# Performance work log

Hardware: AMD Instinct MI355X
Metric: run time of the kernel (lower is better)

## Reference

```python
import jax, jax.numpy as jnp
import numpy as np
import math

SPARSITY = 0.5
EPS = 1e-5


def _quant(x, bit, after_relu):
    # mirrors torch quantize_per_tensor math; straight-through (torch mutates x.data)
    def q(x):
        mx, mn = x.max(), x.min()
        scale = (mx - mn) / (2 ** bit - 1)
        if after_relu:
            ir = jnp.clip(jnp.round(x / scale), 0.0, 2 ** bit - 1)
            return ir * scale
        zp_min = jnp.floor(mn / scale)
        return (jnp.round((x - mn) / scale) + zp_min) * scale
    return x + jax.lax.stop_gradient(q(x) - x)


def _subnet(scores, k):
    # GetSubnet: top-k mask of |scores| with straight-through gradient
    s = jnp.abs(scores)
    flat = s.ravel()
    j = int((1.0 - k) * flat.size)
    order = jnp.argsort(flat)
    mask = jnp.zeros_like(flat).at[order[j:]].set(1.0).reshape(s.shape)
    return jax.lax.stop_gradient(mask - s) + s


def _scale(hw_one, fan_in):
    std = math.sqrt(2.0) / math.sqrt(fan_in * 0.5)
    return hw_one.mean() / std


def _blend_w(scores, sign, hw_one, hw_zero):
    m = _subnet(scores, SPARSITY)
    return sign * (hw_one[0] * m + hw_zero[0] * (1.0 - m))


def _conv(x, w):
    return jax.lax.conv_general_dilated(x, w, (1, 1), 'VALID',
                                        dimension_numbers=('NCHW', 'OIHW', 'NCHW'))


def _maxpool2(x):
    return jax.lax.reduce_window(x, -jnp.inf, jax.lax.max,
                                 (1, 1, 2, 2), (1, 1, 2, 2), 'VALID')


def _bn(x):
    m = x.mean((0, 2, 3), keepdims=True)
    v = x.var((0, 2, 3), keepdims=True)
    return (x - m) / jnp.sqrt(v + EPS)


def setup_inputs() -> dict:
    key = jax.random.key(0)
    ks = jax.random.split(key, 16)
    B = 4096
    shapes = {
        '1': (64, 1, 3, 3),
        '2': (16, 64, 3, 3),
        '3': (128, 400),
        '4': (10, 128),
    }
    inp = {'x': jax.random.normal(ks[0], (B, 1, 28, 28), dtype=jnp.float32)}
    i = 1
    for name, shp in shapes.items():
        inp['scores' + name] = jax.random.normal(ks[i], shp, dtype=jnp.float32); i += 1
        inp['sign' + name] = jnp.sign(jax.random.normal(ks[i], shp, dtype=jnp.float32)); i += 1
        inp['hw' + name + '_one'] = jax.random.uniform(ks[i], (1,) + shp, dtype=jnp.float32); i += 1
        # hw_zero: small "off" conductances
        inp['hw' + name + '_zero'] = 0.05 * jax.random.uniform(jax.random.fold_in(ks[i], 1), (1,) + shp, dtype=jnp.float32)
    inp['qb'] = 8
    return inp


def reference(x, scores1, sign1, hw1_one, hw1_zero,
              scores2, sign2, hw2_one, hw2_zero,
              scores3, sign3, hw3_one, hw3_zero,
              scores4, sign4, hw4_one, hw4_zero, qb):
    x = _maxpool2(x)
    x = _quant(x, qb, False)
    # conv1 (fan_in = 1*3*3 = 9)
    w1 = _blend_w(scores1, sign1, hw1_one, hw1_zero)
    x = _conv(x, w1) / _scale(hw1_one, 9)
    x = jax.nn.relu(_bn(x))
    x = _quant(x, qb, True)
    # conv2 (fan_in = 64*9 = 576)
    w2 = _blend_w(scores2, sign2, hw2_one, hw2_zero)
    x = _conv(x, w2) / _scale(hw2_one, 576)
    x = _maxpool2(x)
    x = jax.nn.relu(_bn(x))
    x = _quant(x, qb, True)
    x = x.reshape(x.shape[0], -1)  # [B, 400]
    # fc1 (fan_in = 400)
    w3 = _blend_w(scores3, sign3, hw3_one, hw3_zero)
    x = (x @ w3.T) / _scale(hw3_one, 400)
    x = jax.nn.relu(x)
    x = _quant(x, qb, True)
    # fc2 (fan_in = 128)
    w4 = _blend_w(scores4, sign4, hw4_one, hw4_zero)
    x = (x @ w4.T) / _scale(hw4_one, 128)
    return jax.nn.log_softmax(x, axis=1)
```

## Files before the change

kernel.cpp:

```cpp
#include <hip/hip_runtime.h>
#include <hip/hip_bf16.h>
#include <math.h>

#define DEV __device__ __forceinline__

constexpr int BATCH = 4096;
constexpr int NBA = 512;
constexpr int NBB = 1024;
constexpr int NBC = 4096;
constexpr int NBE = 512;
constexpr int NBW = 16;

constexpr size_t OFF_POOLED = 0;
constexpr size_t OFF_Y2P = OFF_POOLED + (size_t)BATCH*196;
constexpr size_t OFF_ST1 = OFF_Y2P;
constexpr size_t OFF_H3  = OFF_Y2P + (size_t)BATCH*400;
constexpr size_t OFF_ST2 = OFF_H3;
constexpr size_t OFF_W2  = OFF_H3 + (size_t)BATCH*128;
constexpr size_t OFF_W3  = OFF_W2 + 9216;
constexpr size_t OFF_W4  = OFF_W3 + 51200;
constexpr size_t OFF_WSC = OFF_W4 + 1280;
constexpr size_t OFF_BN1 = OFF_WSC + 4;
constexpr size_t OFF_BN2 = OFF_BN1 + 256;
constexpr size_t OFF_GMM = OFF_BN2 + 64;
constexpr size_t OFF_ONS = OFF_GMM + 8;
constexpr size_t OFF_T   = OFF_ONS + 16;
constexpr size_t OFF_MMA = OFF_T + 4;
constexpr size_t OFF_HIST= OFF_MMA + 1024;
constexpr size_t OFF_W1M = OFF_HIST + 32768;
constexpr size_t OFF_SEL = OFF_W1M + 2048;
constexpr size_t OFF_H2G = OFF_SEL + 8;
constexpr size_t OFF_H3G = OFF_H2G + 4096;

typedef __attribute__((ext_vector_type(8))) short bf16x8;
typedef __attribute__((ext_vector_type(4))) float f32x4;

struct InPtrs {
  const float* x;
  const float* sc[4];
  const float* sg[4];
  const float* on[4];
  const float* ze[4];
  const int* qb;
};

__constant__ const int KW_L[16]  ={0,1,1,2,2,2,2,2,2,2,2,2,2,2,2,3};
__constant__ const int KW_S[16]  ={0,0,1,0,1,2,3,4,5,6,7,8,9,10,11,0};
__constant__ const int KW_NB[4]  ={1,2,12,1};
__constant__ const int KW_N[4]   ={576,9216,51200,1280};
__constant__ const int KW_FAN[4] ={9,576,400,128};
__constant__ const int KW_BW0[4] ={0,1,3,15};
__constant__ const int KW_BW1[4] ={1,3,15,16};

DEV unsigned fenc(float f){ unsigned u=__float_as_uint(f); return (u&0x80000000u)? ~u : (u|0x80000000u); }
DEV float fdec(unsigned e){ return __uint_as_float((e&0x80000000u)? (e&0x7fffffffu) : ~e); }
DEV unsigned short f2bf(float f){ unsigned u=__float_as_uint(f); return (unsigned short)((u + 0x7fffu + ((u>>16)&1u))>>16); }

DEV float blk_sum(float v, float* red, int t){
  red[t]=v; __syncthreads();
  for (int s=128;s>0;s>>=1){ if(t<s) red[t]+=red[t+s]; __syncthreads(); }
  float r=red[0]; __syncthreads();
  return r;
}
DEV float blk_min(float v, float* red, int t){
  red[t]=v; __syncthreads();
  for (int s=128;s>0;s>>=1){ if(t<s) red[t]=fminf(red[t],red[t+s]); __syncthreads(); }
  float r=red[0]; __syncthreads();
  return r;
}
DEV float blk_max(float v, float* red, int t){
  red[t]=v; __syncthreads();
  for (int s=128;s>0;s>>=1){ if(t<s) red[t]=fmaxf(red[t],red[t+s]); __syncthreads(); }
  float r=red[0]; __syncthreads();
  return r;
}

DEV int2 find256(const int* hist, int nbins, int kk, int t, int* suf, int* sh2){
  const int G=nbins>>8;
  const int lo=t*G;
  int g=0;
  for (int b=0;b<G;++b) g+=hist[lo+b];
  suf[t]=g; __syncthreads();
  for (int s=1;s<256;s<<=1){
    int add=(t+s<256)?suf[t+s]:0;
    __syncthreads();
    suf[t]+=add;
    __syncthreads();
  }
  const int S=suf[t];
  const int Snext=(t<255)?suf[t+1]:0;
  if (S>=kk && Snext<kk){
    int c2=Snext;
    for (int b=lo+G-1;b>=lo;--b){
      c2+=hist[b];
      if (c2>=kk){ sh2[0]=b; sh2[1]=kk-(c2-hist[b]); break; }
    }
  }
  __syncthreads();
  int2 r=make_int2(sh2[0],sh2[1]);
  __syncthreads();
  return r;
}

DEV void build_patq(unsigned* PATQ, const unsigned short* qxs, int t){
  for (int pos=t; pos<144; pos+=256){
    int py=(pos*171)>>11;
    int px=pos-py*12;
    const unsigned short* q0=qxs+py*16+px;
    unsigned e0=q0[0],  e1=q0[1],  e2=q0[2];
    unsigned e3=q0[16], e4=q0[17], e5=q0[18];
    unsigned e6=q0[32], e7=q0[33], e8=q0[34];
    *(uint4*)(PATQ+pos*4)      =make_uint4(e0|(e1<<16), e2|(e3<<16), e4|(e5<<16), e6|(e7<<16));
    *(uint4*)(PATQ+(144+pos)*4)=make_uint4(e8, 0u, 0u, 0u);
  }
}

__global__ __launch_bounds__(256) void ka_kernel(InPtrs in, float* __restrict__ ws){
  const int t=threadIdx.x, blk=blockIdx.x;
  __shared__ int h[2048];
  __shared__ float red[256];
  if (blk<NBA){
    if (blk==0){
      unsigned* Z=(unsigned*)(ws+OFF_H2G);
      for (int i=t;i<8192;i+=256) Z[i]=0u;
    }
    const float* x=in.x;
    float* pooled=ws+OFF_POOLED;
    float lmn=3.4e38f, lmx=-3.4e38f;
    if (t<196){
      const int oy=(t*2341)>>15;
      const int ox=t-oy*14;
      const float* xb=x+(size_t)blk*8*784+oy*56+ox*2;
      #pragma unroll
      for (int im=0; im<8; ++im){
        const float* px=xb+im*784;
        float m=fmaxf(fmaxf(px[0],px[1]),fmaxf(px[28],px[29]));
        pooled[(size_t)(blk*8+im)*196+t]=m;
        lmn=fminf(lmn,m); lmx=fmaxf(lmx,m);
      }
    }
    float bmn=blk_min(lmn,red,t);
    float bmx=blk_max(lmx,red,t);
    if (t==0){ ws[OFF_MMA+blk*2]=bmn; ws[OFF_MMA+blk*2+1]=bmx; }
  } else {
    const int bw=blk-NBA;
    const int L=KW_L[bw], s=KW_S[bw], nb=KW_NB[L];
    const int n4=KW_N[L]>>2;
    const int lo=(int)(((long long)n4*s)/nb), hi=(int)(((long long)n4*(s+1))/nb);
    const float4* sc4=(const float4*)in.sc[L];
    const float4* on4=(const float4*)in.on[L];
    for (int i=t;i<2048;i+=256) h[i]=0;
    __syncthreads();
    float onsum=0.f;
    for (int i=lo+t;i<hi;i+=256){
      float4 v=sc4[i];
      atomicAdd(&h[(__float_as_uint(v.x)&0x7fffffffu)>>20],1);
      atomicAdd(&h[(__float_as_uint(v.y)&0x7fffffffu)>>20],1);
      atomicAdd(&h[(__float_as_uint(v.z)&0x7fffffffu)>>20],1);
      atomicAdd(&h[(__float_as_uint(v.w)&0x7fffffffu)>>20],1);
      float4 o=on4[i];
      onsum+=(o.x+o.y)+(o.z+o.w);
    }
    __syncthreads();
    unsigned* GH=(unsigned*)(ws+OFF_HIST);
    for (int i=t;i<2048;i+=256) GH[bw*2048+i]=(unsigned)h[i];
    float S=blk_sum(onsum,red,t);
    if (t==0) ws[OFF_ONS+bw]=S;
  }
}

__global__ __launch_bounds__(256) void kw2a_kernel(float* __restrict__ ws){
  const int t=threadIdx.x, L=blockIdx.x;
  __shared__ int hist[2048];
  __shared__ int suf[256];
  __shared__ int sh2[2];
  __shared__ float redm[256], redx[256];
  if (L==0){
    float a0=ws[OFF_MMA+2*t],       a1=ws[OFF_MMA+2*(t+256)];
    float b0=ws[OFF_MMA+2*t+1],     b1=ws[OFF_MMA+2*(t+256)+1];
    redm[t]=fminf(a0,a1); redx[t]=fmaxf(b0,b1);
    __syncthreads();
    for (int s=128;s>0;s>>=1){
      if (t<s){ redm[t]=fminf(redm[t],redm[t+s]); redx[t]=fmaxf(redx[t],redx[t+s]); }
      __syncthreads();
    }
    unsigned* U=(unsigned*)(ws+OFF_GMM);
    if (t==0){ U[0]=fenc(redm[0]); U[1]=fenc(redx[0]); }
    if (t>=2 && t<8) U[t]=(t&1)? 0u : 0xFFFFFFFFu;
    unsigned* z=(unsigned*)(ws+OFF_W1M);
    for (int i=t;i<2048;i+=256) z[i]=0u;
    __syncthreads();
  }
  const unsigned* GH=(const unsigned*)(ws+OFF_HIST);
  for (int i=t;i<2048;i+=256){
    int s=0;
    for (int bw=KW_BW0[L]; bw<KW_BW1[L]; ++bw) s+=(int)GH[bw*2048+i];
    hist[i]=s;
  }
  __syncthreads();
  int2 f1=find256(hist,2048,KW_N[L]>>1,t,suf,sh2);
  if (t==0){
    unsigned* SEL=(unsigned*)(ws+OFF_SEL);
    SEL[L*2]=(unsigned)f1.x; SEL[L*2+1]=(unsigned)f1.y;
  }
}

__global__ __launch_bounds__(256) void kwp2_kernel(InPtrs in, float* __restrict__ ws){
  const int t=threadIdx.x, bw=blockIdx.x;
  const int L=KW_L[bw], s=KW_S[bw], nb=KW_NB[L];
  const int n4=KW_N[L]>>2;
  const int lo=(int)(((long long)n4*s)/nb), hi=(int)(((long long)n4*(s+1))/nb);
  const unsigned b0=((const unsigned*)(ws+OFF_SEL))[L*2];
  const float4* sc4=(const float4*)in.sc[L];
  unsigned* GH2=(unsigned*)(ws+OFF_H2G)+L*1024;
  for (int i=lo+t;i<hi;i+=256){
    float4 v=sc4[i];
    unsigned ux=__float_as_uint(v.x)&0x7fffffffu;
    unsigned uy=__float_as_uint(v.y)&0x7fffffffu;
    unsigned uz=__float_as_uint(v.z)&0x7fffffffu;
    unsigned uw=__float_as_uint(v.w)&0x7fffffffu;
    if ((ux>>20)==b0) atomicAdd(&GH2[(ux>>10)&1023u],1u);
    if ((uy>>20)==b0) atomicAdd(&GH2[(uy>>10)&1023u],1u);
    if ((uz>>20)==b0) atomicAdd(&GH2[(uz>>10)&1023u],1u);
    if ((uw>>20)==b0) atomicAdd(&GH2[(uw>>10)&1023u],1u);
  }
}

__global__ __launch_bounds__(256) void kwp3_kernel(InPtrs in, float* __restrict__ ws){
  const int t=threadIdx.x, bw=blockIdx.x;
  const int L=KW_L[bw], s=KW_S[bw], nb=KW_NB[L];
  const int n4=KW_N[L]>>2;
  const int lo=(int)(((long long)n4*s)/nb), hi=(int)(((long long)n4*(s+1))/nb);
  const unsigned* SEL=(const unsigned*)(ws+OFF_SEL);
  const unsigned b0=SEL[L*2]; const int r1=(int)SEL[L*2+1];
  __shared__ int hist[1024];
  __shared__ int suf[256];
  __shared__ int sh2[2];
  const unsigned* GH2=(const unsigned*)(ws+OFF_H2G)+L*1024;
  for (int i=t;i<1024;i+=256) hist[i]=(int)GH2[i];
  __syncthreads();
  int2 f2=find256(hist,1024,r1,t,suf,sh2);
  const unsigned pre=(b0<<10)|(unsigned)f2.x;
  const float4* sc4=(const float4*)in.sc[L];
  unsigned* GH3=(unsigned*)(ws+OFF_H3G)+L*1024;
  for (int i=lo+t;i<hi;i+=256){
    float4 v=sc4[i];
    unsigned ux=__float_as_uint(v.x)&0x7fffffffu;
    unsigned uy=__float_as_uint(v.y)&0x7fffffffu;
    unsigned uz=__float_as_uint(v.z)&0x7fffffffu;
    unsigned uw=__float_as_uint(v.w)&0x7fffffffu;
    if ((ux>>10)==pre) atomicAdd(&GH3[ux&1023u],1u);
    if ((uy>>10)==pre) atomicAdd(&GH3[uy&1023u],1u);
    if ((uz>>10)==pre) atomicAdd(&GH3[uz&1023u],1u);
    if ((uw>>10)==pre) atomicAdd(&GH3[uw&1023u],1u);
  }
}

__global__ __launch_bounds__(256) void kw3_kernel(InPtrs in, float* __restrict__ ws){
  const int t=threadIdx.x, bw=blockIdx.x;
  const int L=KW_L[bw], s=KW_S[bw], nb=KW_NB[L];
  const int n4=KW_N[L]>>2;
  const int lo=(int)(((long long)n4*s)/nb), hi=(int)(((long long)n4*(s+1))/nb);
  const unsigned* SEL=(const unsigned*)(ws+OFF_SEL);
  const unsigned b0=SEL[L*2]; const int r1=(int)SEL[L*2+1];
  __shared__ int hist[1024];
  __shared__ int suf[256];
  __shared__ int sh2[2];
  const unsigned* GH2=(const unsigned*)(ws+OFF_H2G)+L*1024;
  for (int i=t;i<1024;i+=256) hist[i]=(int)GH2[i];
  __syncthreads();
  int2 f2=find256(hist,1024,r1,t,suf,sh2);
  const unsigned pre=(b0<<10)|(unsigned)f2.x;
  const int r2=f2.y;
  __syncthreads();
  const unsigned* GH3=(const unsigned*)(ws+OFF_H3G)+L*1024;
  for (int i=t;i<1024;i+=256) hist[i]=(int)GH3[i];
  __syncthreads();
  int2 f3=find256(hist,1024,r2,t,suf,sh2);
  const unsigned T=(pre<<10)|(unsigned)f3.x;
  if (s==0 && t==0){
    float os=0.f;
    for (int b=KW_BW0[L]; b<KW_BW1[L]; ++b) os+=ws[OFF_ONS+b];
    ws[OFF_WSC+L]=(os/(float)KW_N[L])*sqrtf((float)KW_FAN[L])*0.5f;
  }
  const float4* sc4=(const float4*)in.sc[L];
  const float4* sg4=(const float4*)in.sg[L];
  const float4* on4=(const float4*)in.on[L];
  const float4* ze4=(const float4*)in.ze[L];
  float* wout=ws+OFF_W4;
  unsigned* W3Fu=(unsigned*)(ws+OFF_W3);
  unsigned short* W1F=(unsigned short*)(ws+OFF_W1M);
  unsigned short* W2F=(unsigned short*)(ws+OFF_W2);
  for (int i4=lo+t;i4<hi;i4+=256){
    float4 sv4=sc4[i4], g=sg4[i4], o=on4[i4], z=ze4[i4];
    float sv[4]={sv4.x,sv4.y,sv4.z,sv4.w}, gv[4]={g.x,g.y,g.z,g.w};
    float ov[4]={o.x,o.y,o.z,o.w}, zv[4]={z.x,z.y,z.z,z.w};
    #pragma unroll
    for (int j=0;j<4;++j){
      int i=i4*4+j;
      unsigned u=__float_as_uint(sv[j])&0x7fffffffu;
      float w=gv[j]*((u>=T)? ov[j] : zv[j]);
      if (L==0){
        int oc=i/9; int k=i-oc*9;
        int ocT=oc>>4, ocL=oc&15, quad=k>>3, kj=k&7;
        unsigned short hb=f2bf(w);
        float lo2=w-__uint_as_float((unsigned)hb<<16);
        W1F[((((ocT*2+0)*4+quad)*16+ocL)<<3)+kj]=hb;
        W1F[((((ocT*2+1)*4+quad)*16+ocL)<<3)+kj]=f2bf(lo2);
      } else if (L==1){
        int oc=i/576; int r=i-oc*576; int ic=r/9; int kp=r-ic*9;
        int ss=ic>>5, rem=ic&31, quad=rem>>3, kj=rem&7;
        unsigned short hb=f2bf(w);
        float lo2=w-__uint_as_float((unsigned)hb<<16);
        W2F[(((((kp*2+ss)*2+0)*4+quad)*16+oc)<<3)+kj]=hb;
        W2F[(((((kp*2+ss)*2+1)*4+quad)*16+oc)<<3)+kj]=f2bf(lo2);
      } else if (L==2){
        int oc=i/400; int kk=i-oc*400;
        unsigned short hb=f2bf(w);
        float lo2=w-__uint_as_float((unsigned)hb<<16);
        unsigned short lb=f2bf(lo2);
        int ct=oc>>4, l15=oc&15;
        unsigned idx=((unsigned)((kk>>4)*8+ct)*64u + (unsigned)(((kk>>2)&3)*16+l15))*4u + (unsigned)(kk&3);
        W3Fu[idx]=(unsigned)hb | ((unsigned)lb<<16);
      } else {
        wout[i]=w;
      }
    }
  }
}

__global__ __launch_bounds__(256) void kb_kernel(InPtrs in, const float* __restrict__ wsr, float* __restrict__ wsw){
  const int t=threadIdx.x, blk=blockIdx.x;
  __shared__ unsigned short qxs[256];
  __shared__ __align__(16) unsigned PAT[2304];
  __shared__ float xw[1024];
  const float* pooled=wsr+OFF_POOLED;
  const unsigned* U=(const unsigned*)(wsr+OFF_GMM);
  const float mn0=fdec(U[0]);
  const float mx0=fdec(U[1]);
  const float lvf=(float)((1<<in.qb[0])-1);
  const float s0=(mx0-mn0)/lvf, inv_s0=1.0f/s0, zp0=floorf(mn0/s0);
  const float sv=s0/wsr[OFF_WSC+0];
  const int w=t>>6, lane=t&63, l15=lane&15, quad=lane>>4;
  const unsigned short* W1F=(const unsigned short*)(wsr+OFF_W1M);
  bf16x8 bh[4], bl[4];
  #pragma unroll
  for (int ocT=0; ocT<4; ++ocT){
    bh[ocT]=*(const bf16x8*)(W1F+(((ocT*2+0)*64+lane)<<3));
    bl[ocT]=*(const bf16x8*)(W1F+(((ocT*2+1)*64+lane)<<3));
  }
  for (int i=1152+t; i<2304; i+=256) PAT[i]=0u;
  float sum[4], sq[4], mn[4], mx[4];
  #pragma unroll
  for (int i=0;i<4;++i){ sum[i]=0.f; sq[i]=0.f; mn[i]=3.4e38f; mx[i]=-3.4e38f; }
  for (int img=0; img<4; ++img){
    if (t<224){
      int row=t>>4, col=t&15;
      float q=0.f;
      if (col<14){ float xx=pooled[(size_t)(blk*4+img)*196+row*14+col]; q=rintf((xx-mn0)*inv_s0)+zp0; }
      qxs[t]=(unsigned short)(__float_as_uint(q)>>16);
    }
    __syncthreads();
    build_patq(PAT,qxs,t);
    __syncthreads();
    const unsigned short* PATu=(const unsigned short*)PAT;
    #pragma unroll
    for (int ocT=0; ocT<4; ++ocT){
      for (int tl=w; tl<9; tl+=4){
        bf16x8 a=*(const bf16x8*)(PATu+((quad*144+tl*16+l15)<<3));
        f32x4 acc=(f32x4){0.f,0.f,0.f,0.f};
        acc=__builtin_amdgcn_mfma_f32_16x16x32_bf16(a,bh[ocT],acc,0,0,0);
        acc=__builtin_amdgcn_mfma_f32_16x16x32_bf16(a,bl[ocT],acc,0,0,0);
        #pragma unroll
        for (int r=0;r<4;++r){
          float v=acc[r];
          sum[ocT]+=v; sq[ocT]=fmaf(v,v,sq[ocT]);
          mn[ocT]=fminf(mn[ocT],v); mx[ocT]=fmaxf(mx[ocT],v);
        }
      }
    }
    __syncthreads();
  }
  #pragma unroll
  for (int ocT=0; ocT<4; ++ocT){
    float s=sum[ocT], q2=sq[ocT], a=mn[ocT], b=mx[ocT];
    #pragma unroll
    for (int d=16;d<64;d<<=1){
      s+=__shfl_xor(s,d);
      q2+=__shfl_xor(q2,d);
      a=fminf(a,__shfl_xor(a,d));
      b=fmaxf(b,__shfl_xor(b,d));
    }
    if (quad==0){
      float* p=xw+((w*4+ocT)*16+l15)*4;
      p[0]=s; p[1]=q2; p[2]=a; p[3]=b;
    }
  }
  __syncthreads();
  if (t<64){
    float s=0.f,q2=0.f,a=3.4e38f,b=-3.4e38f;
    #pragma unroll
    for (int w2=0;w2<4;++w2){
      const float* p=xw+((w2*4+(t>>4))*16+(t&15))*4;
      s+=p[0]; q2+=p[1]; a=fminf(a,p[2]); b=fmaxf(b,p[3]);
    }
    float* p=wsw+OFF_ST1+((size_t)t*NBB+blk)*4;
    p[0]=s*sv; p[1]=q2*sv*sv; p[2]=a*sv; p[3]=b*sv;
  }
}

__global__ __launch_bounds__(256) void kstat_kernel(const float* __restrict__ wsr, float* __restrict__ wsw,
                                                    unsigned long long inoff, int nparts, float Nf,
                                                    unsigned long long outoff, int mmslot){
  const int c=blockIdx.x, t=threadIdx.x;
  __shared__ float red[256];
  const float* p=wsr+inoff+(size_t)c*nparts*4;
  float sum=0.f,sq=0.f,mn=3.4e38f,mx=-3.4e38f;
  for (int i=t;i<nparts;i+=256){
    sum+=p[i*4]; sq+=p[i*4+1];
    mn=fminf(mn,p[i*4+2]); mx=fmaxf(mx,p[i*4+3]);
  }
  float S=blk_sum(sum,red,t);
  float Q=blk_sum(sq,red,t);
  float MN=blk_min(mn,red,t);
  float MX=blk_max(mx,red,t);
  if (t==0){
    float mean=S/Nf;
    float var=fmaxf(Q/Nf-mean*mean,0.f);
    float sd=sqrtf(var+1e-5f);
    float* o=wsw+outoff+c*4;
    float tmn=(MN-mean)/sd, tmx=(MX-mean)/sd;
    o[0]=mean; o[1]=sd; o[2]=tmn; o[3]=tmx;
    unsigned* U=(unsigned*)(wsw+OFF_GMM);
    atomicMin(&U[mmslot],fenc(tmn));
    atomicMax(&U[mmslot+1],fenc(tmx));
  }
}

__global__ __launch_bounds__(256) void kc_kernel(InPtrs in, const float* __restrict__ wsr, float* __restrict__ wsw){
  const int t=threadIdx.x, blk=blockIdx.x;
  __shared__ unsigned short qxs[256];
  __shared__ __align__(16) unsigned PATBUF[3328];
  __shared__ __align__(16) unsigned short actA[144*88];
  __shared__ float sA2[64], sB2[64];
  unsigned* PAT=PATBUF;
  float (*c2sP)[16][104]=(float(*)[16][104])PATBUF;
  const float* pooled=wsr+OFF_POOLED;
  const unsigned* U=(const unsigned*)(wsr+OFF_GMM);
  const float mn0=fdec(U[0]);
  const float mx0=fdec(U[1]);
  const float rmn=fdec(U[2]);
  const float rmx=fdec(U[3]);
  const float lvf=(float)((1<<in.qb[0])-1);
  const float s0=(mx0-mn0)/lvf, inv_s0=1.0f/s0, zp0=floorf(mn0/s0);
  const float s1w=wsr[OFF_WSC+0], s2w=wsr[OFF_WSC+1];
  const float s2=(fmaxf(rmx,0.f)-fmaxf(rmn,0.f))/lvf;
  const float inv_s2=1.0f/s2;
  const float g2=s2/s2w;
  if (t<64){
    float m=wsr[OFF_BN1+t*4], sd=wsr[OFF_BN1+t*4+1];
    sA2[t]=s0/(s1w*sd)*inv_s2;
    sB2[t]=(-m/sd)*inv_s2;
  }
  if (t<224){
    int row=t>>4, col=t&15;
    float q=0.f;
    if (col<14){ float xx=pooled[(size_t)blk*196+row*14+col]; q=rintf((xx-mn0)*inv_s0)+zp0; }
    qxs[t]=(unsigned short)(__float_as_uint(q)>>16);
  }
  for (int i=1152+t; i<2304; i+=256) PAT[i]=0u;
  __syncthreads();
  build_patq(PAT,qxs,t);
  __syncthreads();
  const int w=t>>6, lane=t&63;
  const int l15=lane&15, quad=lane>>4;
  {
    const unsigned short* W1F=(const unsigned short*)(wsr+OFF_W1M);
    const unsigned short* PATu=(const unsigned short*)PAT;
    #pragma unroll
    for (int ocT=0; ocT<4; ++ocT){
      bf16x8 bh=*(const bf16x8*)(W1F+(((ocT*2+0)*64+lane)<<3));
      bf16x8 bl=*(const bf16x8*)(W1F+(((ocT*2+1)*64+lane)<<3));
      const int oc0=ocT*16+quad*4;
      const float a20=sA2[oc0],   b20=sB2[oc0];
      const float a21=sA2[oc0+1], b21=sB2[oc0+1];
      const float a22=sA2[oc0+2], b22=sB2[oc0+2];
      const float a23=sA2[oc0+3], b23=sB2[oc0+3];
      for (int tl=w; tl<9; tl+=4){
        bf16x8 a=*(const bf16x8*)(PATu+((quad*144+tl*16+l15)<<3));
        f32x4 acc=(f32x4){0.f,0.f,0.f,0.f};
        acc=__builtin_amdgcn_mfma_f32_16x16x32_bf16(bh,a,acc,0,0,0);
        acc=__builtin_amdgcn_mfma_f32_16x16x32_bf16(bl,a,acc,0,0,0);
        const int pos=tl*16+l15;
        float f0=fminf(rintf(fmaxf(fmaf(acc[0],a20,b20),0.f)),lvf);
        float f1=fminf(rintf(fmaxf(fmaf(acc[1],a21,b21),0.f)),lvf);
        float f2v=fminf(rintf(fmaxf(fmaf(acc[2],a22,b22),0.f)),lvf);
        float f3=fminf(rintf(fmaxf(fmaf(acc[3],a23,b23),0.f)),lvf);
        unsigned w0=(__float_as_uint(f0)>>16)|((__float_as_uint(f1)>>16)<<16);
        unsigned w1=(__float_as_uint(f2v)>>16)|((__float_as_uint(f3)>>16)<<16);
        *(uint2*)(actA+pos*88+oc0)=make_uint2(w0,w1);
      }
    }
  }
  __syncthreads();
  {
    const int wm=w>>1, wk=w&1;
    const int k0=wk?5:0, nK=wk?4:5;
    const int nT2=wm?3:4;
    const unsigned short* W2F=(const unsigned short*)(wsr+OFF_W2);
    int abase[4];
    #pragma unroll
    for (int i=0;i<4;++i){
      int tau=wm*4+i;
      int posb=tau*16+l15;
      int pc=posb>99?99:posb;
      int py=pc/10, px=pc-py*10;
      abase[i]=(py*12+px)*176+quad*16;
    }
    f32x4 acc[4];
    acc[0]=(f32x4){0.f,0.f,0.f,0.f};
    acc[1]=(f32x4){0.f,0.f,0.f,0.f};
    acc[2]=(f32x4){0.f,0.f,0.f,0.f};
    acc[3]=(f32x4){0.f,0.f,0.f,0.f};
    const char* actB=(const char*)actA;
    #pragma unroll
    for (int kk=0;kk<5;++kk){
      if (kk<nK){
        int kykx=k0+kk;
        int ky=(kykx*11)>>5;
        int kx=kykx-ky*3;
        int co=(ky*12+kx)*176;
        #pragma unroll
        for (int s=0;s<2;++s){
          bf16x8 bh=*(const bf16x8*)(W2F+((((kykx*2+s)*2+0)*64+lane)<<3));
          bf16x8 bl=*(const bf16x8*)(W2F+((((kykx*2+s)*2+1)*64+lane)<<3));
          #pragma unroll
          for (int i=0;i<4;++i){
            if (i<nT2){
              bf16x8 a=*(const bf16x8*)(actB+abase[i]+co+s*64);
              acc[i]=__builtin_amdgcn_mfma_f32_16x16x32_bf16(a,bh,acc[i],0,0,0);
              acc[i]=__builtin_amdgcn_mfma_f32_16x16x32_bf16(a,bl,acc[i],0,0,0);
            }
          }
        }
      }
    }
    #pragma unroll
    for (int i=0;i<4;++i){
      if (i<nT2){
        int pos4=(wm*4+i)*16+quad*4;
        if (pos4<100){
          float4* dst=(float4*)&c2sP[wk][l15][pos4];
          *dst=make_float4(acc[i].x*g2,acc[i].y*g2,acc[i].z*g2,acc[i].w*g2);
        }
      }
    }
  }
  __syncthreads();
  {
    const int ch=t>>4, g=t&15;
    const float* cc0=&c2sP[0][ch][0];
    const float* cc1=&c2sP[1][ch][0];
    float sum=0.f,sq=0.f,mn=3.4e38f,mx=-3.4e38f;
    #pragma unroll
    for (int it=0;it<2;++it){
      int j=g+it*16;
      if (j<25){
        int py=(j*52)>>8;
        int px=j-py*5;
        int base=py*20+px*2;
        float2 p0=*(const float2*)(cc0+base);
        float2 p1=*(const float2*)(cc0+base+10);
        float2 q0=*(const float2*)(cc1+base);
        float2 q1=*(const float2*)(cc1+base+10);
        float a0=p0.x+q0.x, a1=p0.y+q0.y;
        float b0=p1.x+q1.x, b1=p1.y+q1.y;
        float v=fmaxf(fmaxf(a0,a1),fmaxf(b0,b1));
        wsw[OFF_Y2P+(size_t)blk*400+ch*25+j]=v;
        sum+=v; sq=fmaf(v,v,sq); mn=fminf(mn,v); mx=fmaxf(mx,v);
      }
    }
    #pragma unroll
    for (int d=1;d<16;d<<=1){
      sum+=__shfl_xor(sum,d);
      sq +=__shfl_xor(sq,d);
      mn=fminf(mn,__shfl_xor(mn,d));
      mx=fmaxf(mx,__shfl_xor(mx,d));
    }
    if (g==0){
      float* p=wsw+OFF_ST2+((size_t)ch*NBC+blk)*4;
      p[0]=sum; p[1]=sq; p[2]=mn; p[3]=mx;
    }
  }
}

__global__ __launch_bounds__(256) void ke_kernel(InPtrs in, const float* __restrict__ wsr, float* __restrict__ wsw){
  const int t=threadIdx.x, blk=blockIdx.x;
  __shared__ __align__(16) unsigned short xs[16*808];
  __shared__ float sm[16], sisd[16];
  __shared__ float rwn[4], rwx[4];
  const unsigned* U=(const unsigned*)(wsr+OFF_GMM);
  const float lvf=(float)((1<<in.qb[0])-1);
  const float rmn=fdec(U[4]);
  const float rmx=fdec(U[5]);
  if (t<16){ sm[t]=wsr[OFF_BN2+t*4]; sisd[t]=1.0f/wsr[OFF_BN2+t*4+1]; }
  const float s3=(fmaxf(rmx,0.f)-fmaxf(rmn,0.f))/lvf;
  const float inv_s3=1.0f/s3;
  const float inv_s3w=1.0f/wsr[OFF_WSC+2];
  const int b0=(blk>>1)*16;
  __syncthreads();
  {
    const int img=t>>4, tg=t&15;
    const float* yrow=wsr+OFF_Y2P+(size_t)(b0+img)*400;
    unsigned* xsu=(unsigned*)xs;
    for (int n=0;n<25;++n){
      int k=n*16+tg;
      int ch=(k*5243)>>17;
      float y=yrow[k];
      float r=fmaxf((y-sm[ch])*sisd[ch],0.f);
      float q=fminf(rintf(r*inv_s3),lvf);
      unsigned qb=__float_as_uint(q)>>16;
      xsu[img*404+k]=qb|(qb<<16);
    }
  }
  __syncthreads();
  const int w=t>>6, lane=t&63, l15=lane&15, quad=lane>>4;
  const int ct=(blk&1)*4+w;
  const bf16x8* Wf=(const bf16x8*)(wsr+OFF_W3);
  const unsigned short* arow=xs+l15*808;
  f32x4 acc=(f32x4){0.f,0.f,0.f,0.f};
  #pragma unroll 5
  for (int kt=0;kt<25;++kt){
    bf16x8 a=*(const bf16x8*)(arow+kt*32+quad*8);
    bf16x8 b=Wf[(kt*8+ct)*64+lane];
    acc=__builtin_amdgcn_mfma_f32_16x16x32_bf16(a,b,acc,0,0,0);
  }
  const float scale=s3*inv_s3w;
  float hmn=3.4e38f,hmx=-3.4e38f;
  #pragma unroll
  for (int r=0;r<4;++r){
    float h=fmaxf(acc[r]*scale,0.f);
    wsw[OFF_H3+(size_t)(b0+quad*4+r)*128+ct*16+l15]=h;
    hmn=fminf(hmn,h); hmx=fmaxf(hmx,h);
  }
  #pragma unroll
  for (int d=1;d<64;d<<=1){
    hmn=fminf(hmn,__shfl_xor(hmn,d));
    hmx=fmaxf(hmx,__shfl_xor(hmx,d));
  }
  if (lane==0){ rwn[w]=hmn; rwx[w]=hmx; }
  __syncthreads();
  if (t==0){
    float mn=fminf(fminf(rwn[0],rwn[1]),fminf(rwn[2],rwn[3]));
    float mx=fmaxf(fmaxf(rwx[0],rwx[1]),fmaxf(rwx[2],rwx[3]));
    float* p=wsw+OFF_MMA+(size_t)blk*2;
    p[0]=mn; p[1]=mx;
  }
}

__global__ __launch_bounds__(256) void kf_kernel(InPtrs in, const float* __restrict__ wsr, float* __restrict__ out){
  const int t=threadIdx.x, blk=blockIdx.x;
  __shared__ float w4s[1280];
  __shared__ float redn[256], redxs[256];
  const float lvf=(float)((1<<in.qb[0])-1);
  for (int i=t;i<1280;i+=256) w4s[i]=wsr[OFF_W4+i];
  {
    const float* mmp=wsr+OFF_MMA;
    float mn=3.4e38f, mx=-3.4e38f;
    for (int i=t;i<NBE;i+=256){
      mn=fminf(mn,mmp[2*i]);
      mx=fmaxf(mx,mmp[2*i+1]);
    }
    redn[t]=mn; redxs[t]=mx;
    __syncthreads();
    for (int s=128;s>0;s>>=1){
      if (t<s){ redn[t]=fminf(redn[t],redn[t+s]); redxs[t]=fmaxf(redxs[t],redxs[t+s]); }
      __syncthreads();
    }
  }
  const float hmn=redn[0];
  const float hmx=redxs[0];
  const float s4=(hmx-hmn)/lvf;
  const float inv_s4=1.0f/s4;
  const float inv_s4w=1.0f/wsr[OFF_WSC+3];
  const int row=blk*64+(t>>2), l4=t&3;
  const float4* hr4=(const float4*)(wsr+OFF_H3+(size_t)row*128);
  float acc[10];
  #pragma unroll
  for (int j=0;j<10;++j) acc[j]=0.f;
  #pragma unroll 2
  for (int j=0;j<8;++j){
    float4 v=hr4[l4*8+j];
    int kb=(l4*8+j)*4;
    float q0=fminf(rintf(v.x*inv_s4),lvf)*s4;
    float q1=fminf(rintf(v.y*inv_s4),lvf)*s4;
    float q2=fminf(rintf(v.z*inv_s4),lvf)*s4;
    float q3=fminf(rintf(v.w*inv_s4),lvf)*s4;
    #pragma unroll
    for (int o=0;o<10;++o){
      const float* wr=w4s+o*128+kb;
      acc[o]=fmaf(q0,wr[0],acc[o]);
      acc[o]=fmaf(q1,wr[1],acc[o]);
      acc[o]=fmaf(q2,wr[2],acc[o]);
      acc[o]=fmaf(q3,wr[3],acc[o]);
    }
  }
  #pragma unroll
  for (int o=0;o<10;++o){
    acc[o]+=__shfl_xor(acc[o],1);
    acc[o]+=__shfl_xor(acc[o],2);
  }
  if (l4==0){
    float mx=-3.4e38f;
    #pragma unroll
    for (int o=0;o<10;++o){ acc[o]*=inv_s4w; mx=fmaxf(mx,acc[o]); }
    float se=0.f;
    #pragma unroll
    for (int o=0;o<10;++o) se+=expf(acc[o]-mx);
    const float ls=logf(se);
    #pragma unroll
    for (int o=0;o<10;++o) out[row*10+o]=acc[o]-mx-ls;
  }
}

extern "C" void kernel_launch(void* const* d_in, const int* in_sizes, int n_in,
                              void* d_out, int out_size, void* d_ws, size_t ws_size,
                              hipStream_t stream){
  (void)in_sizes; (void)n_in; (void)out_size; (void)ws_size;
  InPtrs P;
  P.x=(const float*)d_in[0];
  for (int l=0;l<4;++l){
    P.sc[l]=(const float*)d_in[1+l*4];
    P.sg[l]=(const float*)d_in[2+l*4];
    P.on[l]=(const float*)d_in[3+l*4];
    P.ze[l]=(const float*)d_in[4+l*4];
  }
  P.qb=(const int*)d_in[17];
  float* ws=(float*)d_ws;

  hipLaunchKernelGGL(ka_kernel,   dim3(NBA+NBW), dim3(256), 0, stream, P, ws);
  hipLaunchKernelGGL(kw2a_kernel, dim3(4),       dim3(256), 0, stream, ws);
  hipLaunchKernelGGL(kwp2_kernel, dim3(NBW),     dim3(256), 0, stream, P, ws);
  hipLaunchKernelGGL(kwp3_kernel, dim3(NBW),     dim3(256), 0, stream, P, ws);
  hipLaunchKernelGGL(kw3_kernel,  dim3(NBW),     dim3(256), 0, stream, P, ws);
  hipLaunchKernelGGL(kb_kernel,   dim3(NBB),     dim3(256), 0, stream, P, ws, ws);
  hipLaunchKernelGGL(kstat_kernel, dim3(64), dim3(256), 0, stream, ws, ws,
                     (unsigned long long)OFF_ST1, NBB, 4096.f*144.f, (unsigned long long)OFF_BN1, 2);
  hipLaunchKernelGGL(kc_kernel,   dim3(NBC),     dim3(256), 0, stream, P, ws, ws);
  hipLaunchKernelGGL(kstat_kernel, dim3(16), dim3(256), 0, stream, ws, ws,
                     (unsigned long long)OFF_ST2, NBC, 4096.f*25.f, (unsigned long long)OFF_BN2, 4);
  hipLaunchKernelGGL(ke_kernel,   dim3(NBE),     dim3(256), 0, stream, P, ws, ws);
  hipLaunchKernelGGL(kf_kernel,   dim3(64),      dim3(256), 0, stream, P, ws, (float*)d_out);
}
```

Before: 230.4 us.

## Merge selection into histogram pass and coarsen per-block work in conv/fc kernels

Folds the small kw2a kernel, which reduces the histogram and finds the top-k bucket, into kwp2, so that every kwp2 block recomputes the bucket selection locally and one launch is removed. kb now handles 8 images per block, kc handles 2 images per block in a loop, and ke uses 512 threads to cover all 8 column tiles of a 16-row batch. The aim is to cut launch overhead and per-block setup such as weight loads and stat writes. The cost is fewer blocks and therefore less parallelism, plus redundant histogram reduction work in each kwp2 block.

New measurement: 242.6 us. 5.3% more time.

```diff
diff --git a/kernel.cpp b/kernel.cpp
--- a/kernel.cpp
+++ b/kernel.cpp
@@ -6,9 +6,9 @@
 
 constexpr int BATCH = 4096;
 constexpr int NBA = 512;
-constexpr int NBB = 1024;
-constexpr int NBC = 4096;
-constexpr int NBE = 512;
+constexpr int NBB = 512;
+constexpr int NBC = 2048;
+constexpr int NBE = 256;
 constexpr int NBW = 16;
 
 constexpr size_t OFF_POOLED = 0;
@@ -169,48 +169,46 @@
   }
 }
 
-__global__ __launch_bounds__(256) void kw2a_kernel(float* __restrict__ ws){
-  const int t=threadIdx.x, L=blockIdx.x;
+__global__ __launch_bounds__(256) void kwp2_kernel(InPtrs in, float* __restrict__ ws){
+  const int t=threadIdx.x, bw=blockIdx.x;
   __shared__ int hist[2048];
   __shared__ int suf[256];
   __shared__ int sh2[2];
   __shared__ float redm[256], redx[256];
-  if (L==0){
+  const int L=KW_L[bw], s=KW_S[bw], nb=KW_NB[L];
+  const int n4=KW_N[L]>>2;
+  const int lo=(int)(((long long)n4*s)/nb), hi=(int)(((long long)n4*(s+1))/nb);
+  if (bw==0){
     float a0=ws[OFF_MMA+2*t],       a1=ws[OFF_MMA+2*(t+256)];
-    float b0=ws[OFF_MMA+2*t+1],     b1=ws[OFF_MMA+2*(t+256)+1];
-    redm[t]=fminf(a0,a1); redx[t]=fmaxf(b0,b1);
-    __syncthreads();
-    for (int s=128;s>0;s>>=1){
-      if (t<s){ redm[t]=fminf(redm[t],redm[t+s]); redx[t]=fmaxf(redx[t],redx[t+s]); }
+    float b0v=ws[OFF_MMA+2*t+1],    b1v=ws[OFF_MMA+2*(t+256)+1];
+    redm[t]=fminf(a0,a1); redx[t]=fmaxf(b0v,b1v);
+    __syncthreads();
+    for (int st=128;st>0;st>>=1){
+      if (t<st){ redm[t]=fminf(redm[t],redm[t+st]); redx[t]=fmaxf(redx[t],redx[t+st]); }
       __syncthreads();
     }
     unsigned* U=(unsigned*)(ws+OFF_GMM);
     if (t==0){ U[0]=fenc(redm[0]); U[1]=fenc(redx[0]); }
     if (t>=2 && t<8) U[t]=(t&1)? 0u : 0xFFFFFFFFu;
+    __syncthreads();
+  }
+  if (bw==15){
     unsigned* z=(unsigned*)(ws+OFF_W1M);
     for (int i=t;i<2048;i+=256) z[i]=0u;
-    __syncthreads();
   }
   const unsigned* GH=(const unsigned*)(ws+OFF_HIST);
   for (int i=t;i<2048;i+=256){
-    int s=0;
-    for (int bw=KW_BW0[L]; bw<KW_BW1[L]; ++bw) s+=(int)GH[bw*2048+i];
-    hist[i]=s;
+    int sm=0;
+    for (int b2=KW_BW0[L]; b2<KW_BW1[L]; ++b2) sm+=(int)GH[b2*2048+i];
+    hist[i]=sm;
   }
   __syncthreads();
   int2 f1=find256(hist,2048,KW_N[L]>>1,t,suf,sh2);
-  if (t==0){
+  const unsigned b0=(unsigned)f1.x;
+  if (s==0 && t==0){
     unsigned* SEL=(unsigned*)(ws+OFF_SEL);
     SEL[L*2]=(unsigned)f1.x; SEL[L*2+1]=(unsigned)f1.y;
   }
-}
-
-__global__ __launch_bounds__(256) void kwp2_kernel(InPtrs in, float* __restrict__ ws){
-  const int t=threadIdx.x, bw=blockIdx.x;
-  const int L=KW_L[bw], s=KW_S[bw], nb=KW_NB[L];
-  const int n4=KW_N[L]>>2;
-  const int lo=(int)(((long long)n4*s)/nb), hi=(int)(((long long)n4*(s+1))/nb);
-  const unsigned b0=((const unsigned*)(ws+OFF_SEL))[L*2];
   const float4* sc4=(const float4*)in.sc[L];
   unsigned* GH2=(unsigned*)(ws+OFF_H2G)+L*1024;
   for (int i=lo+t;i<hi;i+=256){
@@ -353,11 +351,11 @@
   float sum[4], sq[4], mn[4], mx[4];
   #pragma unroll
   for (int i=0;i<4;++i){ sum[i]=0.f; sq[i]=0.f; mn[i]=3.4e38f; mx[i]=-3.4e38f; }
-  for (int img=0; img<4; ++img){
+  for (int img=0; img<8; ++img){
     if (t<224){
       int row=t>>4, col=t&15;
       float q=0.f;
-      if (col<14){ float xx=pooled[(size_t)(blk*4+img)*196+row*14+col]; q=rintf((xx-mn0)*inv_s0)+zp0; }
+      if (col<14){ float xx=pooled[(size_t)(blk*8+img)*196+row*14+col]; q=rintf((xx-mn0)*inv_s0)+zp0; }
       qxs[t]=(unsigned short)(__float_as_uint(q)>>16);
     }
     __syncthreads();
@@ -462,143 +460,148 @@
     sA2[t]=s0/(s1w*sd)*inv_s2;
     sB2[t]=(-m/sd)*inv_s2;
   }
-  if (t<224){
-    int row=t>>4, col=t&15;
-    float q=0.f;
-    if (col<14){ float xx=pooled[(size_t)blk*196+row*14+col]; q=rintf((xx-mn0)*inv_s0)+zp0; }
-    qxs[t]=(unsigned short)(__float_as_uint(q)>>16);
-  }
-  for (int i=1152+t; i<2304; i+=256) PAT[i]=0u;
-  __syncthreads();
-  build_patq(PAT,qxs,t);
-  __syncthreads();
   const int w=t>>6, lane=t&63;
   const int l15=lane&15, quad=lane>>4;
-  {
-    const unsigned short* W1F=(const unsigned short*)(wsr+OFF_W1M);
-    const unsigned short* PATu=(const unsigned short*)PAT;
-    #pragma unroll
-    for (int ocT=0; ocT<4; ++ocT){
-      bf16x8 bh=*(const bf16x8*)(W1F+(((ocT*2+0)*64+lane)<<3));
-      bf16x8 bl=*(const bf16x8*)(W1F+(((ocT*2+1)*64+lane)<<3));
-      const int oc0=ocT*16+quad*4;
-      const float a20=sA2[oc0],   b20=sB2[oc0];
-      const float a21=sA2[oc0+1], b21=sB2[oc0+1];
-      const float a22=sA2[oc0+2], b22=sB2[oc0+2];
-      const float a23=sA2[oc0+3], b23=sB2[oc0+3];
-      for (int tl=w; tl<9; tl+=4){
-        bf16x8 a=*(const bf16x8*)(PATu+((quad*144+tl*16+l15)<<3));
-        f32x4 acc=(f32x4){0.f,0.f,0.f,0.f};
-        acc=__builtin_amdgcn_mfma_f32_16x16x32_bf16(bh,a,acc,0,0,0);
-        acc=__builtin_amdgcn_mfma_f32_16x16x32_bf16(bl,a,acc,0,0,0);
-        const int pos=tl*16+l15;
-        float f0=fminf(rintf(fmaxf(fmaf(acc[0],a20,b20),0.f)),lvf);
-        float f1=fminf(rintf(fmaxf(fmaf(acc[1],a21,b21),0.f)),lvf);
-        float f2v=fminf(rintf(fmaxf(fmaf(acc[2],a22,b22),0.f)),lvf);
-        float f3=fminf(rintf(fmaxf(fmaf(acc[3],a23,b23),0.f)),lvf);
-        unsigned w0=(__float_as_uint(f0)>>16)|((__float_as_uint(f1)>>16)<<16);
-        unsigned w1=(__float_as_uint(f2v)>>16)|((__float_as_uint(f3)>>16)<<16);
-        *(uint2*)(actA+pos*88+oc0)=make_uint2(w0,w1);
-      }
-    }
-  }
-  __syncthreads();
-  {
-    const int wm=w>>1, wk=w&1;
-    const int k0=wk?5:0, nK=wk?4:5;
-    const int nT2=wm?3:4;
-    const unsigned short* W2F=(const unsigned short*)(wsr+OFF_W2);
-    int abase[4];
-    #pragma unroll
-    for (int i=0;i<4;++i){
-      int tau=wm*4+i;
-      int posb=tau*16+l15;
-      int pc=posb>99?99:posb;
-      int py=pc/10, px=pc-py*10;
-      abase[i]=(py*12+px)*176+quad*16;
-    }
-    f32x4 acc[4];
-    acc[0]=(f32x4){0.f,0.f,0.f,0.f};
-    acc[1]=(f32x4){0.f,0.f,0.f,0.f};
-    acc[2]=(f32x4){0.f,0.f,0.f,0.f};
-    acc[3]=(f32x4){0.f,0.f,0.f,0.f};
-    const char* actB=(const char*)actA;
-    #pragma unroll
-    for (int kk=0;kk<5;++kk){
-      if (kk<nK){
-        int kykx=k0+kk;
-        int ky=(kykx*11)>>5;
-        int kx=kykx-ky*3;
-        int co=(ky*12+kx)*176;
-        #pragma unroll
-        for (int s=0;s<2;++s){
-          bf16x8 bh=*(const bf16x8*)(W2F+((((kykx*2+s)*2+0)*64+lane)<<3));
-          bf16x8 bl=*(const bf16x8*)(W2F+((((kykx*2+s)*2+1)*64+lane)<<3));
+  const int pch=t>>4, pg=t&15;
+  float psum=0.f,psq=0.f,pmn=3.4e38f,pmx=-3.4e38f;
+  for (int img=0; img<2; ++img){
+    for (int i=1152+t; i<2304; i+=256) PAT[i]=0u;
+    if (t<224){
+      int row=t>>4, col=t&15;
+      float q=0.f;
+      if (col<14){ float xx=pooled[(size_t)(blk*2+img)*196+row*14+col]; q=rintf((xx-mn0)*inv_s0)+zp0; }
+      qxs[t]=(unsigned short)(__float_as_uint(q)>>16);
+    }
+    __syncthreads();
+    build_patq(PAT,qxs,t);
+    __syncthreads();
+    {
+      const unsigned short* W1F=(const unsigned short*)(wsr+OFF_W1M);
+      const unsigned short* PATu=(const unsigned short*)PAT;
+      #pragma unroll
+      for (int ocT=0; ocT<4; ++ocT){
+        bf16x8 bh=*(const bf16x8*)(W1F+(((ocT*2+0)*64+lane)<<3));
+        bf16x8 bl=*(const bf16x8*)(W1F+(((ocT*2+1)*64+lane)<<3));
+        const int oc0=ocT*16+quad*4;
+        const float a20=sA2[oc0],   b20=sB2[oc0];
+        const float a21=sA2[oc0+1], b21=sB2[oc0+1];
+        const float a22=sA2[oc0+2], b22=sB2[oc0+2];
+        const float a23=sA2[oc0+3], b23=sB2[oc0+3];
+        for (int tl=w; tl<9; tl+=4){
+          bf16x8 a=*(const bf16x8*)(PATu+((quad*144+tl*16+l15)<<3));
+          f32x4 acc=(f32x4){0.f,0.f,0.f,0.f};
+          acc=__builtin_amdgcn_mfma_f32_16x16x32_bf16(bh,a,acc,0,0,0);
+          acc=__builtin_amdgcn_mfma_f32_16x16x32_bf16(bl,a,acc,0,0,0);
+          const int pos=tl*16+l15;
+          float f0=fminf(rintf(fmaxf(fmaf(acc[0],a20,b20),0.f)),lvf);
+          float f1=fminf(rintf(fmaxf(fmaf(acc[1],a21,b21),0.f)),lvf);
+          float f2v=fminf(rintf(fmaxf(fmaf(acc[2],a22,b22),0.f)),lvf);
+          float f3=fminf(rintf(fmaxf(fmaf(acc[3],a23,b23),0.f)),lvf);
+          unsigned w0=(__float_as_uint(f0)>>16)|((__float_as_uint(f1)>>16)<<16);
+          unsigned w1=(__float_as_uint(f2v)>>16)|((__float_as_uint(f3)>>16)<<16);
+          *(uint2*)(actA+pos*88+oc0)=make_uint2(w0,w1);
+        }
+      }
+    }
+    __syncthreads();
+    {
+      const int wm=w>>1, wk=w&1;
+      const int k0=wk?5:0, nK=wk?4:5;
+      const int nT2=wm?3:4;
+      const unsigned short* W2F=(const unsigned short*)(wsr+OFF_W2);
+      int abase[4];
+      #pragma unroll
+      for (int i=0;i<4;++i){
+        int tau=wm*4+i;
+        int posb=tau*16+l15;
+        int pc=posb>99?99:posb;
+        int py=pc/10, px=pc-py*10;
+        abase[i]=(py*12+px)*176+quad*16;
+      }
+      f32x4 acc[4];
+      acc[0]=(f32x4){0.f,0.f,0.f,0.f};
+      acc[1]=(f32x4){0.f,0.f,0.f,0.f};
+      acc[2]=(f32x4){0.f,0.f,0.f,0.f};
+      acc[3]=(f32x4){0.f,0.f,0.f,0.f};
+      const char* actB=(const char*)actA;
+      #pragma unroll
+      for (int kk=0;kk<5;++kk){
+        if (kk<nK){
+          int kykx=k0+kk;
+          int ky=(kykx*11)>>5;
+          int kx=kykx-ky*3;
+          int co=(ky*12+kx)*176;
           #pragma unroll
-          for (int i=0;i<4;++i){
-            if (i<nT2){
-              bf16x8 a=*(const bf16x8*)(actB+abase[i]+co+s*64);
-              acc[i]=__builtin_amdgcn_mfma_f32_16x16x32_bf16(a,bh,acc[i],0,0,0);
-              acc[i]=__builtin_amdgcn_mfma_f32_16x16x32_bf16(a,bl,acc[i],0,0,0);
+          for (int s=0;s<2;++s){
+            bf16x8 bh=*(const bf16x8*)(W2F+((((kykx*2+s)*2+0)*64+lane)<<3));
+            bf16x8 bl=*(const bf16x8*)(W2F+((((kykx*2+s)*2+1)*64+lane)<<3));
+            #pragma unroll
+            for (int i=0;i<4;++i){
+              if (i<nT2){
+                bf16x8 a=*(const bf16x8*)(actB+abase[i]+co+s*64);
+                acc[i]=__builtin_amdgcn_mfma_f32_16x16x32_bf16(a,bh,acc[i],0,0,0);
+                acc[i]=__builtin_amdgcn_mfma_f32_16x16x32_bf16(a,bl,acc[i],0,0,0);
+              }
             }
           }
         }
       }
-    }
-    #pragma unroll
-    for (int i=0;i<4;++i){
-      if (i<nT2){
-        int pos4=(wm*4+i)*16+quad*4;
-        if (pos4<100){
-          float4* dst=(float4*)&c2sP[wk][l15][pos4];
-          *dst=make_float4(acc[i].x*g2,acc[i].y*g2,acc[i].z*g2,acc[i].w*g2);
+      #pragma unroll
+      for (int i=0;i<4;++i){
+        if (i<nT2){
+          int pos4=(wm*4+i)*16+quad*4;
+          if (pos4<100){
+            float4* dst=(float4*)&c2sP[wk][l15][pos4];
+            *dst=make_float4(acc[i].x*g2,acc[i].y*g2,acc[i].z*g2,acc[i].w*g2);
+          }
         }
       }
     }
-  }
-  __syncthreads();
+    __syncthreads();
+    {
+      const float* cc0=&c2sP[0][pch][0];
+      const float* cc1=&c2sP[1][pch][0];
+      #pragma unroll
+      for (int it=0;it<2;++it){
+        int j=pg+it*16;
+        if (j<25){
+          int py=(j*52)>>8;
+          int px=j-py*5;
+          int base=py*20+px*2;
+          float2 p0=*(const float2*)(cc0+base);
+          float2 p1=*(const float2*)(cc0+base+10);
+          float2 q0=*(const float2*)(cc1+base);
+          float2 q1=*(const float2*)(cc1+base+10);
+          float a0=p0.x+q0.x, a1=p0.y+q0.y;
+          float b0=p1.x+q1.x, b1=p1.y+q1.y;
+          float v=fmaxf(fmaxf(a0,a1),fmaxf(b0,b1));
+          wsw[OFF_Y2P+(size_t)(blk*2+img)*400+pch*25+j]=v;
+          psum+=v; psq=fmaf(v,v,psq); pmn=fminf(pmn,v); pmx=fmaxf(pmx,v);
+        }
+      }
+    }
+    __syncthreads();
+  }
   {
-    const int ch=t>>4, g=t&15;
-    const float* cc0=&c2sP[0][ch][0];
-    const float* cc1=&c2sP[1][ch][0];
-    float sum=0.f,sq=0.f,mn=3.4e38f,mx=-3.4e38f;
-    #pragma unroll
-    for (int it=0;it<2;++it){
-      int j=g+it*16;
-      if (j<25){
-        int py=(j*52)>>8;
-        int px=j-py*5;
-        int base=py*20+px*2;
-        float2 p0=*(const float2*)(cc0+base);
-        float2 p1=*(const float2*)(cc0+base+10);
-        float2 q0=*(const float2*)(cc1+base);
-        float2 q1=*(const float2*)(cc1+base+10);
-        float a0=p0.x+q0.x, a1=p0.y+q0.y;
-        float b0=p1.x+q1.x, b1=p1.y+q1.y;
-        float v=fmaxf(fmaxf(a0,a1),fmaxf(b0,b1));
-        wsw[OFF_Y2P+(size_t)blk*400+ch*25+j]=v;
-        sum+=v; sq=fmaf(v,v,sq); mn=fminf(mn,v); mx=fmaxf(mx,v);
-      }
-    }
     #pragma unroll
     for (int d=1;d<16;d<<=1){
-      sum+=__shfl_xor(sum,d);
-      sq +=__shfl_xor(sq,d);
-      mn=fminf(mn,__shfl_xor(mn,d));
-      mx=fmaxf(mx,__shfl_xor(mx,d));
-    }
-    if (g==0){
-      float* p=wsw+OFF_ST2+((size_t)ch*NBC+blk)*4;
-      p[0]=sum; p[1]=sq; p[2]=mn; p[3]=mx;
-    }
-  }
-}
-
-__global__ __launch_bounds__(256) void ke_kernel(InPtrs in, const float* __restrict__ wsr, float* __restrict__ wsw){
+      psum+=__shfl_xor(psum,d);
+      psq +=__shfl_xor(psq,d);
+      pmn=fminf(pmn,__shfl_xor(pmn,d));
+      pmx=fmaxf(pmx,__shfl_xor(pmx,d));
+    }
+    if (pg==0){
+      float* p=wsw+OFF_ST2+((size_t)pch*NBC+blk)*4;
+      p[0]=psum; p[1]=psq; p[2]=pmn; p[3]=pmx;
+    }
+  }
+}
+
+__global__ __launch_bounds__(512) void ke_kernel(InPtrs in, const float* __restrict__ wsr, float* __restrict__ wsw){
   const int t=threadIdx.x, blk=blockIdx.x;
   __shared__ __align__(16) unsigned short xs[16*808];
   __shared__ float sm[16], sisd[16];
-  __shared__ float rwn[4], rwx[4];
+  __shared__ float rwn[8], rwx[8];
   const unsigned* U=(const unsigned*)(wsr+OFF_GMM);
   const float lvf=(float)((1<<in.qb[0])-1);
   const float rmn=fdec(U[4]);
@@ -607,25 +610,27 @@
   const float s3=(fmaxf(rmx,0.f)-fmaxf(rmn,0.f))/lvf;
   const float inv_s3=1.0f/s3;
   const float inv_s3w=1.0f/wsr[OFF_WSC+2];
-  const int b0=(blk>>1)*16;
+  const int b0=blk*16;
   __syncthreads();
   {
-    const int img=t>>4, tg=t&15;
+    const int img=t>>5, tg=t&31;
     const float* yrow=wsr+OFF_Y2P+(size_t)(b0+img)*400;
     unsigned* xsu=(unsigned*)xs;
-    for (int n=0;n<25;++n){
-      int k=n*16+tg;
-      int ch=(k*5243)>>17;
-      float y=yrow[k];
-      float r=fmaxf((y-sm[ch])*sisd[ch],0.f);
-      float q=fminf(rintf(r*inv_s3),lvf);
-      unsigned qb=__float_as_uint(q)>>16;
-      xsu[img*404+k]=qb|(qb<<16);
+    for (int n=0;n<13;++n){
+      int k=n*32+tg;
+      if (k<400){
+        int ch=(k*5243)>>17;
+        float y=yrow[k];
+        float r=fmaxf((y-sm[ch])*sisd[ch],0.f);
+        float q=fminf(rintf(r*inv_s3),lvf);
+        unsigned qb=__float_as_uint(q)>>16;
+        xsu[img*404+k]=qb|(qb<<16);
+      }
     }
   }
   __syncthreads();
   const int w=t>>6, lane=t&63, l15=lane&15, quad=lane>>4;
-  const int ct=(blk&1)*4+w;
+  const int ct=w;
   const bf16x8* Wf=(const bf16x8*)(wsr+OFF_W3);
   const unsigned short* arow=xs+l15*808;
   f32x4 acc=(f32x4){0.f,0.f,0.f,0.f};
@@ -651,8 +656,9 @@
   if (lane==0){ rwn[w]=hmn; rwx[w]=hmx; }
   __syncthreads();
   if (t==0){
-    float mn=fminf(fminf(rwn[0],rwn[1]),fminf(rwn[2],rwn[3]));
-    float mx=fmaxf(fmaxf(rwx[0],rwx[1]),fmaxf(rwx[2],rwx[3]));
+    float mn=rwn[0], mx=rwx[0];
+    #pragma unroll
+    for (int i=1;i<8;++i){ mn=fminf(mn,rwn[i]); mx=fmaxf(mx,rwx[i]); }
     float* p=wsw+OFF_MMA+(size_t)blk*2;
     p[0]=mn; p[1]=mx;
   }
@@ -667,9 +673,9 @@
   {
     const float* mmp=wsr+OFF_MMA;
     float mn=3.4e38f, mx=-3.4e38f;
-    for (int i=t;i<NBE;i+=256){
-      mn=fminf(mn,mmp[2*i]);
-      mx=fmaxf(mx,mmp[2*i+1]);
+    if (t<NBE){
+      mn=mmp[2*t];
+      mx=mmp[2*t+1];
     }
     redn[t]=mn; redxs[t]=mx;
     __syncthreads();
@@ -739,7 +745,6 @@
   float* ws=(float*)d_ws;
 
   hipLaunchKernelGGL(ka_kernel,   dim3(NBA+NBW), dim3(256), 0, stream, P, ws);
-  hipLaunchKernelGGL(kw2a_kernel, dim3(4),       dim3(256), 0, stream, ws);
   hipLaunchKernelGGL(kwp2_kernel, dim3(NBW),     dim3(256), 0, stream, P, ws);
   hipLaunchKernelGGL(kwp3_kernel, dim3(NBW),     dim3(256), 0, stream, P, ws);
   hipLaunchKernelGGL(kw3_kernel,  dim3(NBW),     dim3(256), 0, stream, P, ws);
@@ -749,6 +754,6 @@
   hipLaunchKernelGGL(kc_kernel,   dim3(NBC),     dim3(256), 0, stream, P, ws, ws);
   hipLaunchKernelGGL(kstat_kernel, dim3(16), dim3(256), 0, stream, ws, ws,
                      (unsigned long long)OFF_ST2, NBC, 4096.f*25.f, (unsigned long long)OFF_BN2, 4);
-  hipLaunchKernelGGL(ke_kernel,   dim3(NBE),     dim3(256), 0, stream, P, ws, ws);
+  hipLaunchKernelGGL(ke_kernel,   dim3(NBE),     dim3(512), 0, stream, P, ws, ws);
   hipLaunchKernelGGL(kf_kernel,   dim3(64),      dim3(256), 0, stream, P, ws, (float*)d_out);
 }
```
